# Kernel tuning notes

Hardware: AMD Instinct MI355X
Metric: run time of the kernel (lower is better)

Reference implementation:

```python
import jax, jax.numpy as jnp
import numpy as np

B, S, D, H = 4, 2048, 1024, 16
HD = D // H  # head dim = 64


def setup_inputs() -> dict:
    key = jax.random.key(0)
    k1, k2, k3 = jax.random.split(key, 3)
    scale = 1.0 / np.sqrt(D).astype(np.float32)
    x = jax.random.normal(k1, (B, S, D), dtype=jnp.float32)
    # q/k slices of nn.MultiheadAttention's in_proj (v and out_proj never
    # influence the returned values since x_t is discarded by forward)
    wq = jax.random.normal(k2, (D, D), dtype=jnp.float32) * scale
    wk = jax.random.normal(k3, (D, D), dtype=jnp.float32) * scale
    bq = jnp.zeros((D,), dtype=jnp.float32)
    bk = jnp.zeros((D,), dtype=jnp.float32)
    # 8 contiguous scale blocks of 256 tokens; last boundary == S
    scales_idx = (jnp.arange(1, 9, dtype=jnp.int64) * (S // 8))
    return {"x": x, "wq": wq, "wk": wk, "bq": bq, "bk": bk,
            "scales_idx": scales_idx}


def reference(x, wq, wk, bq, bk, scales_idx):
    b, s, d = x.shape
    # project q, k and split heads: [B, H, S, HD]
    q = (x @ wq.T + bq).reshape(b, s, H, HD).transpose(0, 2, 1, 3)
    k = (x @ wk.T + bk).reshape(b, s, H, HD).transpose(0, 2, 1, 3)
    inv_sqrt_hd = jnp.asarray(1.0 / np.sqrt(HD), dtype=x.dtype)
    scores = jnp.einsum('bhqd,bhkd->bhqk', q, k) * inv_sqrt_hd  # [B,H,S,S]
    # block-diagonal mask: token i belongs to the block whose right boundary
    # is the first scales_idx entry strictly greater than i
    pos = jnp.arange(s)
    seg = jnp.searchsorted(scales_idx, pos, side='right')  # [S]
    allowed = seg[:, None] == seg[None, :]                  # [S,S] bool
    scores = jnp.where(allowed[None, None], scores, -jnp.inf)
    w = jax.nn.softmax(scores, axis=-1)  # every row has >=1 allowed entry
    weights_attn = jnp.mean(w, axis=1)   # average over heads -> [B,S,S]
    return (x, weights_attn)
```

## Files before the change

kernel.cpp:

```cpp
#include <hip/hip_runtime.h>
#include <hip/hip_bf16.h>
#include <math.h>

#define BB 4
#define SS 2048
#define DD 1024
#define HH 16
#define HD 64
#define MM (BB*SS)
#define NN (2*DD)
#define BK 64
#define NKT 16

typedef __attribute__((ext_vector_type(8))) short short8;
typedef __attribute__((ext_vector_type(4))) float f32x4;
typedef unsigned short ushort_t;

__device__ __forceinline__ void gload16(const void* g, void* l) {
    __builtin_amdgcn_global_load_lds((const __attribute__((address_space(1))) unsigned int*)g,
                                     (__attribute__((address_space(3))) unsigned int*)l,
                                     16, 0, 0);
}

__global__ __launch_bounds__(256)
void copy_cast(const float* __restrict__ x, float* __restrict__ out_x,
               __hip_bfloat16* __restrict__ xb, int n8)
{
    int i = blockIdx.x * 256 + threadIdx.x;
    if (i >= n8) return;
    const f32x4* s = (const f32x4*)x + (size_t)i * 2;
    f32x4 a = s[0], b = s[1];
    f32x4* o = (f32x4*)out_x + (size_t)i * 2;
    __builtin_nontemporal_store(a, o);
    __builtin_nontemporal_store(b, o + 1);
    __hip_bfloat16 tmp[8];
    tmp[0] = __float2bfloat16(a.x); tmp[1] = __float2bfloat16(a.y);
    tmp[2] = __float2bfloat16(a.z); tmp[3] = __float2bfloat16(a.w);
    tmp[4] = __float2bfloat16(b.x); tmp[5] = __float2bfloat16(b.y);
    tmp[6] = __float2bfloat16(b.z); tmp[7] = __float2bfloat16(b.w);
    *(float4*)&xb[(size_t)i * 8] = *(float4*)tmp;
}

__global__ __launch_bounds__(256)
void cast_w(const float* __restrict__ wq, const float* __restrict__ wk,
            __hip_bfloat16* __restrict__ wb)
{
    const int half = (DD * DD) / 8;
    int i = blockIdx.x * 256 + threadIdx.x;
    if (i >= 2 * half) return;
    const float* src = (i < half) ? wq : wk;
    int j = (i < half) ? i : i - half;
    const float4* s = (const float4*)src + (size_t)j * 2;
    float4 a = s[0], b = s[1];
    __hip_bfloat16 tmp[8];
    tmp[0] = __float2bfloat16(a.x); tmp[1] = __float2bfloat16(a.y);
    tmp[2] = __float2bfloat16(a.z); tmp[3] = __float2bfloat16(a.w);
    tmp[4] = __float2bfloat16(b.x); tmp[5] = __float2bfloat16(b.y);
    tmp[6] = __float2bfloat16(b.z); tmp[7] = __float2bfloat16(b.w);
    *(float4*)&wb[(size_t)i * 8] = *(float4*)tmp;
}

__device__ __forceinline__ void stage_A(const ushort_t* __restrict__ xb, ushort_t* Ab,
                                        int m0, int kt, int mh, int wv, int lane)
{
    #pragma unroll
    for (int it = 0; it < 2; ++it) {
        int rl0 = it * 64 + wv * 8;
        int r0 = (rl0 & 63) + ((rl0 >> 6) << 7) + mh * 64;
        int r  = r0 + (lane >> 3);
        int gch = (lane & 7) ^ (r & 7);
        gload16(xb + (size_t)(m0 + r) * DD + kt + gch * 8, Ab + r0 * 64);
    }
}

__device__ __forceinline__ void stage_Bt(const ushort_t* __restrict__ wb, ushort_t* Bb,
                                         int n0, int kt, int nh, int wv, int lane)
{
    #pragma unroll
    for (int it = 0; it < 2; ++it) {
        int rl0 = it * 64 + wv * 8;
        int r0 = (rl0 & 31) + ((rl0 >> 5) << 6) + nh * 32;
        int r  = r0 + (lane >> 3);
        int gch = (lane & 7) ^ (r & 7);
        gload16(wb + (size_t)(n0 + r) * DD + kt + gch * 8, Bb + r0 * 64);
    }
}

__global__ __launch_bounds__(512, 2)
void proj_mfma(const ushort_t* __restrict__ xb, const ushort_t* __restrict__ wb,
               const float* __restrict__ bq, const float* __restrict__ bk,
               __hip_bfloat16* __restrict__ Qb, __hip_bfloat16* __restrict__ Kb)
{
    __shared__ __align__(16) ushort_t As[2][256 * BK];
    __shared__ __align__(16) ushort_t Bs[2][256 * BK];

    const int t = threadIdx.x;
    const int wv = t >> 6, lane = t & 63, quad = lane >> 4, l15 = lane & 15;
    const int wr = wv >> 2, wc = wv & 3;
    const int m0 = blockIdx.x * 256, n0 = blockIdx.y * 256;

    f32x4 acc[8][4];
    #pragma unroll
    for (int mt = 0; mt < 8; ++mt)
        #pragma unroll
        for (int nt = 0; nt < 4; ++nt) acc[mt][nt] = (f32x4){0.f, 0.f, 0.f, 0.f};

    stage_Bt(wb, Bs[0], n0, 0, 0, wv, lane);
    stage_A (xb, As[0], m0, 0, 0, wv, lane);
    stage_A (xb, As[0], m0, 0, 1, wv, lane);
    stage_Bt(wb, Bs[0], n0, 0, 1, wv, lane);
    stage_Bt(wb, Bs[1], n0, BK, 0, wv, lane);
    stage_A (xb, As[1], m0, BK, 0, wv, lane);
    asm volatile("s_waitcnt vmcnt(4)" ::: "memory");
    __builtin_amdgcn_s_barrier();

    #pragma unroll 1
    for (int tt = 0; tt < NKT; ++tt) {
        ushort_t* Ac = As[tt & 1];
        ushort_t* Bc = Bs[tt & 1];
        ushort_t* An = As[(tt & 1) ^ 1];
        ushort_t* Bn = Bs[(tt & 1) ^ 1];
        short8 a[8][2], b0[2][2], b1[2][2];

        #pragma unroll
        for (int mt = 0; mt < 8; ++mt)
            #pragma unroll
            for (int ks = 0; ks < 2; ++ks) {
                int r = wr * 128 + mt * 16 + l15;
                int sl = r * 8 + ((ks * 4 + quad) ^ (r & 7));
                a[mt][ks] = *(const short8*)&Ac[sl * 8];
            }
        #pragma unroll
        for (int nt = 0; nt < 2; ++nt)
            #pragma unroll
            for (int ks = 0; ks < 2; ++ks) {
                int r = wc * 64 + nt * 16 + l15;
                int sl = r * 8 + ((ks * 4 + quad) ^ (r & 7));
                b0[nt][ks] = *(const short8*)&Bc[sl * 8];
            }
        if (tt + 1 < NKT) {
            stage_A (xb, An, m0, (tt + 1) * BK, 1, wv, lane);
            stage_Bt(wb, Bn, n0, (tt + 1) * BK, 1, wv, lane);
        }
        __builtin_amdgcn_s_barrier();
        asm volatile("s_waitcnt lgkmcnt(0)" ::: "memory");
        __builtin_amdgcn_sched_barrier(0);
        __builtin_amdgcn_s_setprio(1);
        #pragma unroll
        for (int mt = 0; mt < 8; ++mt)
            #pragma unroll
            for (int nt = 0; nt < 2; ++nt)
                #pragma unroll
                for (int ks = 0; ks < 2; ++ks)
                    acc[mt][nt] = __builtin_amdgcn_mfma_f32_16x16x32_bf16(
                        a[mt][ks], b0[nt][ks], acc[mt][nt], 0, 0, 0);
        __builtin_amdgcn_s_setprio(0);
        __builtin_amdgcn_sched_barrier(0);
        __builtin_amdgcn_s_barrier();

        #pragma unroll
        for (int nt = 0; nt < 2; ++nt)
            #pragma unroll
            for (int ks = 0; ks < 2; ++ks) {
                int r = wc * 64 + 32 + nt * 16 + l15;
                int sl = r * 8 + ((ks * 4 + quad) ^ (r & 7));
                b1[nt][ks] = *(const short8*)&Bc[sl * 8];
            }
        if (tt + 2 < NKT) {
            stage_Bt(wb, Bc, n0, (tt + 2) * BK, 0, wv, lane);
            stage_A (xb, Ac, m0, (tt + 2) * BK, 0, wv, lane);
        }
        asm volatile("s_waitcnt lgkmcnt(0)" ::: "memory");
        __builtin_amdgcn_sched_barrier(0);
        __builtin_amdgcn_s_setprio(1);
        #pragma unroll
        for (int mt = 0; mt < 8; ++mt)
            #pragma unroll
            for (int nt = 0; nt < 2; ++nt)
                #pragma unroll
                for (int ks = 0; ks < 2; ++ks)
                    acc[mt][2 + nt] = __builtin_amdgcn_mfma_f32_16x16x32_bf16(
                        a[mt][ks], b1[nt][ks], acc[mt][2 + nt], 0, 0, 0);
        __builtin_amdgcn_s_setprio(0);
        __builtin_amdgcn_sched_barrier(0);
        if (tt < NKT - 2)       asm volatile("s_waitcnt vmcnt(4)" ::: "memory");
        else if (tt == NKT - 2) asm volatile("s_waitcnt vmcnt(0)" ::: "memory");
        __builtin_amdgcn_s_barrier();
    }

    const bool isQ = (n0 < DD);
    const float* bias = isQ ? bq : bk;
    __hip_bfloat16* outp = isQ ? Qb : Kb;
    const int nc0 = (isQ ? n0 : n0 - DD) + wc * 64;
    #pragma unroll
    for (int nt = 0; nt < 4; ++nt) {
        const int nc = nc0 + nt * 16 + l15;
        const float bv = bias[nc];
        #pragma unroll
        for (int mt = 0; mt < 8; ++mt)
            #pragma unroll
            for (int reg = 0; reg < 4; ++reg) {
                int m = m0 + wr * 128 + mt * 16 + quad * 4 + reg;
                outp[(size_t)m * DD + nc] = __float2bfloat16(acc[mt][nt][reg] + bv);
            }
    }
}

__global__ __launch_bounds__(256, 1)
void attn_block(const ushort_t* __restrict__ Qb, const ushort_t* __restrict__ Kb,
                const int* __restrict__ scales, float* __restrict__ outw)
{
    __shared__ __align__(16) char smem[147456];
    float (*comb)[256] = (float(*)[256])smem;

    const int bid = blockIdx.x;
    const int rt  = bid >> 5;
    const int blk = bid & 7, bb = (bid >> 3) & 3;
    const int start = blk ? scales[blk - 1] : 0;

    const int t = threadIdx.x;
    const int wv = t >> 6, lane = t & 63, quad = lane >> 4, l15 = lane & 15;
    const int rg = wv & 1, hg = wv >> 1;

    f32x4 accm[16];
    #pragma unroll
    for (int nt = 0; nt < 16; ++nt) accm[nt] = (f32x4){0.f, 0.f, 0.f, 0.f};

    const int qrow0 = start + rt * 32;
    const int brow  = bb * SS;

    auto stageKQ = [&](int i, int buf) {
        #pragma unroll
        for (int half = 0; half < 2; ++half) {
            const int h = half * 8 + i;
            ushort_t* Kl = (ushort_t*)(smem + (size_t)(buf * 2 + half) * 32768);
            ushort_t* Ql = (ushort_t*)(smem + 131072 + (size_t)(buf * 2 + half) * 4096);
            #pragma unroll
            for (int round = 0; round < 8; ++round) {
                int c = round * 256 + t;
                int row = c >> 3, ch = c & 7;
                int gch = ch ^ (row & 7);
                gload16(Kb + (size_t)(brow + start + row) * DD + h * HD + gch * 8,
                        Kl + ((size_t)round * 256 + wv * 64) * 8);
            }
            {
                int row = t >> 3, ch = t & 7;
                int gch = ch ^ (row & 7);
                gload16(Qb + (size_t)(brow + qrow0 + row) * DD + h * HD + gch * 8,
                        Ql + ((size_t)wv * 64) * 8);
            }
        }
    };

    stageKQ(0, 0);

    for (int i = 0; i < 8; ++i) {
        if (i < 7) {
            stageKQ(i + 1, (i + 1) & 1);
            asm volatile("s_waitcnt vmcnt(18)" ::: "memory");
        } else {
            asm volatile("s_waitcnt vmcnt(0)" ::: "memory");
        }
        __builtin_amdgcn_s_barrier();

        const ushort_t* Ks = (const ushort_t*)(smem + (size_t)((i & 1) * 2 + hg) * 32768);
        const ushort_t* Qs = (const ushort_t*)(smem + 131072 + (size_t)((i & 1) * 2 + hg) * 4096);

        short8 af[2];
        #pragma unroll
        for (int ks = 0; ks < 2; ++ks) {
            int qr = rg * 16 + l15;
            int sl = qr * 8 + ((ks * 4 + quad) ^ (qr & 7));
            af[ks] = *(const short8*)&Qs[sl * 8];
        }
        f32x4 sc[16];
        #pragma unroll
        for (int nt = 0; nt < 16; ++nt) {
            sc[nt] = (f32x4){0.f, 0.f, 0.f, 0.f};
            #pragma unroll
            for (int ks = 0; ks < 2; ++ks) {
                int kr = nt * 16 + l15;
                int sl = kr * 8 + ((ks * 4 + quad) ^ (kr & 7));
                short8 bf = *(const short8*)&Ks[sl * 8];
                sc[nt] = __builtin_amdgcn_mfma_f32_16x16x32_bf16(af[ks], bf, sc[nt], 0, 0, 0);
            }
        }
        float rs[4] = {0.f, 0.f, 0.f, 0.f};
        #pragma unroll
        for (int nt = 0; nt < 16; ++nt) {
            #pragma unroll
            for (int r = 0; r < 4; ++r) {
                float p = __expf(sc[nt][r] * 0.125f);
                sc[nt][r] = p;
                rs[r] += p;
            }
        }
        #pragma unroll
        for (int r = 0; r < 4; ++r) {
            #pragma unroll
            for (int off = 1; off < 16; off <<= 1) rs[r] += __shfl_xor(rs[r], off, 64);
            rs[r] = 1.0f / rs[r];
        }
        #pragma unroll
        for (int nt = 0; nt < 16; ++nt)
            #pragma unroll
            for (int r = 0; r < 4; ++r) accm[nt][r] += sc[nt][r] * rs[r];

        __builtin_amdgcn_s_barrier();
    }

    __syncthreads();
    if (hg == 0) {
        #pragma unroll
        for (int nt = 0; nt < 16; ++nt)
            #pragma unroll
            for (int r = 0; r < 4; ++r)
                comb[rg * 16 + quad * 4 + r][nt * 16 + l15] = accm[nt][r];
    }
    __syncthreads();
    if (hg == 1) {
        #pragma unroll
        for (int nt = 0; nt < 16; ++nt)
            #pragma unroll
            for (int r = 0; r < 4; ++r)
                comb[rg * 16 + quad * 4 + r][nt * 16 + l15] += accm[nt][r];
    }
    __syncthreads();

    const float s16 = 1.0f / (float)HH;
    const size_t orow0 = (size_t)bb * SS + qrow0;
    #pragma unroll
    for (int it = 0; it < 64; ++it) {
        int flat = it * 256 + t;
        int row = flat >> 9;
        int col = (flat & 511) * 4;
        f32x4 v = (f32x4){0.f, 0.f, 0.f, 0.f};
        unsigned lc = (unsigned)(col - start);
        if (lc < 256u) {
            const float* c = &comb[row][lc];
            v = (f32x4){c[0] * s16, c[1] * s16, c[2] * s16, c[3] * s16};
        }
        __builtin_nontemporal_store(v, (f32x4*)&outw[(orow0 + row) * SS + col]);
    }
}

extern "C" void kernel_launch(void* const* d_in, const int* in_sizes, int n_in,
                              void* d_out, int out_size, void* d_ws, size_t ws_size,
                              hipStream_t stream)
{
    const float* x  = (const float*)d_in[0];
    const float* wq = (const float*)d_in[1];
    const float* wk = (const float*)d_in[2];
    const float* bq = (const float*)d_in[3];
    const float* bk = (const float*)d_in[4];
    const int* scales = (const int*)d_in[5];

    float* out_x = (float*)d_out;
    float* out_w = out_x + (size_t)BB * SS * DD;

    char* w = (char*)d_ws;
    __hip_bfloat16* xb = (__hip_bfloat16*)(w);
    __hip_bfloat16* wb = (__hip_bfloat16*)(w + 16777216);
    __hip_bfloat16* Qb = (__hip_bfloat16*)(w + 20971520);
    __hip_bfloat16* Kb = (__hip_bfloat16*)(w + 37748736);

    copy_cast<<<4096, 256, 0, stream>>>(x, out_x, xb, (MM * DD) / 8);
    cast_w<<<1024, 256, 0, stream>>>(wq, wk, wb);

    dim3 pgrid(MM / 256, NN / 256);
    proj_mfma<<<pgrid, 512, 0, stream>>>((const ushort_t*)xb, (const ushort_t*)wb,
                                         bq, bk, Qb, Kb);

    attn_block<<<256, 256, 0, stream>>>((const ushort_t*)Qb, (const ushort_t*)Kb,
                                        scales, out_w);
}
```

Before: 205.1 us.

## Split attention across key columns per wave and halve query tile

The block-attention kernel now gives each block 16 query rows and loops over all 16 heads sequentially. The four waves split the 256 key columns, and per-row softmax sums are combined through a small shared-memory reduction. The final head-sum combine buffer is gone, so results are stored straight from registers. Shared memory drops from about 144KB to 74KB, so launch bounds allow 2 blocks per CU and the grid doubles to 512 blocks. In exchange, each K tile is reloaded by twice as many blocks, and every head iteration adds an extra barrier for the row-sum exchange.

```diff
diff --git a/kernel.cpp b/kernel.cpp
--- a/kernel.cpp
+++ b/kernel.cpp
@@ -206,12 +206,11 @@
     }
 }
 
-__global__ __launch_bounds__(256, 1)
+__global__ __launch_bounds__(256, 2)
 void attn_block(const ushort_t* __restrict__ Qb, const ushort_t* __restrict__ Kb,
                 const int* __restrict__ scales, float* __restrict__ outw)
 {
-    __shared__ __align__(16) char smem[147456];
-    float (*comb)[256] = (float(*)[256])smem;
+    __shared__ __align__(16) char smem[65536 + 8192 + 512];
 
     const int bid = blockIdx.x;
     const int rt  = bid >> 5;
@@ -220,128 +219,119 @@
 
     const int t = threadIdx.x;
     const int wv = t >> 6, lane = t & 63, quad = lane >> 4, l15 = lane & 15;
-    const int rg = wv & 1, hg = wv >> 1;
-
-    f32x4 accm[16];
-    #pragma unroll
-    for (int nt = 0; nt < 16; ++nt) accm[nt] = (f32x4){0.f, 0.f, 0.f, 0.f};
-
-    const int qrow0 = start + rt * 32;
+
+    const int qrow0 = start + rt * 16;
     const int brow  = bb * SS;
-
-    auto stageKQ = [&](int i, int buf) {
-        #pragma unroll
-        for (int half = 0; half < 2; ++half) {
-            const int h = half * 8 + i;
-            ushort_t* Kl = (ushort_t*)(smem + (size_t)(buf * 2 + half) * 32768);
-            ushort_t* Ql = (ushort_t*)(smem + 131072 + (size_t)(buf * 2 + half) * 4096);
-            #pragma unroll
-            for (int round = 0; round < 8; ++round) {
-                int c = round * 256 + t;
-                int row = c >> 3, ch = c & 7;
-                int gch = ch ^ (row & 7);
-                gload16(Kb + (size_t)(brow + start + row) * DD + h * HD + gch * 8,
-                        Kl + ((size_t)round * 256 + wv * 64) * 8);
-            }
-            {
-                int row = t >> 3, ch = t & 7;
-                int gch = ch ^ (row & 7);
+    float* rsm = (float*)(smem + 73728);
+
+    f32x4 accm[4];
+    #pragma unroll
+    for (int nt = 0; nt < 4; ++nt) accm[nt] = (f32x4){0.f, 0.f, 0.f, 0.f};
+
+    auto stageH = [&](int h, int buf) {
+        ushort_t* Kl = (ushort_t*)(smem + buf * 32768);
+        #pragma unroll
+        for (int it = 0; it < 8; ++it) {
+            int c = it * 256 + t;
+            int row = c >> 3, ch = c & 7;
+            int gch = ch ^ (row & 7);
+            gload16(Kb + (size_t)(brow + start + row) * DD + h * HD + gch * 8,
+                    Kl + ((size_t)it * 256 + wv * 64) * 8);
+        }
+        ushort_t* Ql = (ushort_t*)(smem + 65536 + buf * 4096);
+        {
+            int c = wv * 32 + (lane & 31);
+            int row = c >> 3, ch = c & 7;
+            int gch = ch ^ (row & 7);
+            if (lane < 32)
                 gload16(Qb + (size_t)(brow + qrow0 + row) * DD + h * HD + gch * 8,
-                        Ql + ((size_t)wv * 64) * 8);
-            }
+                        Ql + ((size_t)wv * 32) * 8);
         }
     };
 
-    stageKQ(0, 0);
-
-    for (int i = 0; i < 8; ++i) {
-        if (i < 7) {
-            stageKQ(i + 1, (i + 1) & 1);
-            asm volatile("s_waitcnt vmcnt(18)" ::: "memory");
+    stageH(0, 0);
+
+    #pragma unroll 1
+    for (int h = 0; h < HH; ++h) {
+        if (h < HH - 1) {
+            stageH(h + 1, (h + 1) & 1);
+            asm volatile("s_waitcnt vmcnt(9)" ::: "memory");
         } else {
             asm volatile("s_waitcnt vmcnt(0)" ::: "memory");
         }
         __builtin_amdgcn_s_barrier();
 
-        const ushort_t* Ks = (const ushort_t*)(smem + (size_t)((i & 1) * 2 + hg) * 32768);
-        const ushort_t* Qs = (const ushort_t*)(smem + 131072 + (size_t)((i & 1) * 2 + hg) * 4096);
+        const ushort_t* Ks = (const ushort_t*)(smem + (h & 1) * 32768);
+        const ushort_t* Qs = (const ushort_t*)(smem + 65536 + (h & 1) * 4096);
 
         short8 af[2];
         #pragma unroll
         for (int ks = 0; ks < 2; ++ks) {
-            int qr = rg * 16 + l15;
-            int sl = qr * 8 + ((ks * 4 + quad) ^ (qr & 7));
+            int r = l15;
+            int sl = r * 8 + ((ks * 4 + quad) ^ (r & 7));
             af[ks] = *(const short8*)&Qs[sl * 8];
         }
-        f32x4 sc[16];
-        #pragma unroll
-        for (int nt = 0; nt < 16; ++nt) {
+        f32x4 sc[4];
+        #pragma unroll
+        for (int nt = 0; nt < 4; ++nt) {
             sc[nt] = (f32x4){0.f, 0.f, 0.f, 0.f};
             #pragma unroll
             for (int ks = 0; ks < 2; ++ks) {
-                int kr = nt * 16 + l15;
+                int kr = wv * 64 + nt * 16 + l15;
                 int sl = kr * 8 + ((ks * 4 + quad) ^ (kr & 7));
                 short8 bf = *(const short8*)&Ks[sl * 8];
                 sc[nt] = __builtin_amdgcn_mfma_f32_16x16x32_bf16(af[ks], bf, sc[nt], 0, 0, 0);
             }
         }
-        float rs[4] = {0.f, 0.f, 0.f, 0.f};
-        #pragma unroll
-        for (int nt = 0; nt < 16; ++nt) {
+        float pr[4] = {0.f, 0.f, 0.f, 0.f};
+        #pragma unroll
+        for (int nt = 0; nt < 4; ++nt)
             #pragma unroll
             for (int r = 0; r < 4; ++r) {
                 float p = __expf(sc[nt][r] * 0.125f);
                 sc[nt][r] = p;
-                rs[r] += p;
-            }
-        }
+                pr[r] += p;
+            }
         #pragma unroll
         for (int r = 0; r < 4; ++r) {
             #pragma unroll
-            for (int off = 1; off < 16; off <<= 1) rs[r] += __shfl_xor(rs[r], off, 64);
-            rs[r] = 1.0f / rs[r];
-        }
-        #pragma unroll
-        for (int nt = 0; nt < 16; ++nt)
-            #pragma unroll
-            for (int r = 0; r < 4; ++r) accm[nt][r] += sc[nt][r] * rs[r];
-
-        __builtin_amdgcn_s_barrier();
-    }
-
-    __syncthreads();
-    if (hg == 0) {
-        #pragma unroll
-        for (int nt = 0; nt < 16; ++nt)
-            #pragma unroll
-            for (int r = 0; r < 4; ++r)
-                comb[rg * 16 + quad * 4 + r][nt * 16 + l15] = accm[nt][r];
-    }
-    __syncthreads();
-    if (hg == 1) {
-        #pragma unroll
-        for (int nt = 0; nt < 16; ++nt)
-            #pragma unroll
-            for (int r = 0; r < 4; ++r)
-                comb[rg * 16 + quad * 4 + r][nt * 16 + l15] += accm[nt][r];
-    }
-    __syncthreads();
+            for (int off = 1; off < 16; off <<= 1) pr[r] += __shfl_xor(pr[r], off, 64);
+        }
+        if (l15 == 0) {
+            #pragma unroll
+            for (int r = 0; r < 4; ++r) rsm[wv * 32 + quad * 4 + r] = pr[r];
+        }
+        __builtin_amdgcn_s_barrier();
+        #pragma unroll
+        for (int r = 0; r < 4; ++r) {
+            int row = quad * 4 + r;
+            float tot = rsm[row] + rsm[32 + row] + rsm[64 + row] + rsm[96 + row];
+            float inv = 1.0f / tot;
+            #pragma unroll
+            for (int nt = 0; nt < 4; ++nt) accm[nt][r] += sc[nt][r] * inv;
+        }
+        __builtin_amdgcn_s_barrier();
+    }
 
     const float s16 = 1.0f / (float)HH;
-    const size_t orow0 = (size_t)bb * SS + qrow0;
-    #pragma unroll
-    for (int it = 0; it < 64; ++it) {
+    const size_t orow0 = (size_t)brow + qrow0;
+    #pragma unroll
+    for (int it = 0; it < 32; ++it) {
         int flat = it * 256 + t;
         int row = flat >> 9;
         int col = (flat & 511) * 4;
-        f32x4 v = (f32x4){0.f, 0.f, 0.f, 0.f};
-        unsigned lc = (unsigned)(col - start);
-        if (lc < 256u) {
-            const float* c = &comb[row][lc];
-            v = (f32x4){c[0] * s16, c[1] * s16, c[2] * s16, c[3] * s16};
-        }
-        __builtin_nontemporal_store(v, (f32x4*)&outw[(orow0 + row) * SS + col]);
-    }
+        if ((unsigned)(col - start) >= 256u) {
+            f32x4 z = (f32x4){0.f, 0.f, 0.f, 0.f};
+            __builtin_nontemporal_store(z, (f32x4*)&outw[(orow0 + row) * SS + col]);
+        }
+    }
+    #pragma unroll
+    for (int nt = 0; nt < 4; ++nt)
+        #pragma unroll
+        for (int r = 0; r < 4; ++r) {
+            size_t off = (orow0 + quad * 4 + r) * SS + start + wv * 64 + nt * 16 + l15;
+            __builtin_nontemporal_store(accm[nt][r] * s16, &outw[off]);
+        }
 }
 
 extern "C" void kernel_launch(void* const* d_in, const int* in_sizes, int n_in,
@@ -371,6 +361,6 @@
     proj_mfma<<<pgrid, 512, 0, stream>>>((const ushort_t*)xb, (const ushort_t*)wb,
                                          bq, bk, Qb, Kb);
 
-    attn_block<<<256, 256, 0, stream>>>((const ushort_t*)Qb, (const ushort_t*)Kb,
+    attn_block<<<512, 256, 0, stream>>>((const ushort_t*)Qb, (const ushort_t*)Kb,
                                         scales, out_w);
 }
```

New measurement: 210.1 us. 1.02x slower.
